# Optimization experiments

Measured on AMD Instinct MI355X. Metric: run time of the kernel, lower is better.

The kernel has to match this reference:

```python
import jax, jax.numpy as jnp
import numpy as np

K_NBR = 64  # max_num_neighbors in radius()
M1, M2, M3 = 2048, 512, 512  # fps sample counts: 4096*0.5, 2048*0.25, 512*1.0
R1, R2, R3 = 0.2, 0.4, 1.0


def _fps_idx(pos, m):
    # Furthest point sampling, deterministic start at index 0. pos: [N,3] -> idx [m]
    d2 = jnp.sum((pos - pos[0]) ** 2, axis=-1)  # [N]

    def step(min_d2, _):
        nxt = jnp.argmax(min_d2).astype(jnp.int32)
        min_d2 = jnp.minimum(min_d2, jnp.sum((pos - pos[nxt]) ** 2, axis=-1))
        return min_d2, nxt

    _, rest = jax.lax.scan(step, d2, None, length=m - 1)
    return jnp.concatenate([jnp.zeros((1,), jnp.int32), rest])


def _ball_query(pos_src, pos_q, r, k):
    # Nearest up-to-k neighbors within radius r. Returns idx [M,k], valid mask [M,k].
    d2 = (jnp.sum(pos_q ** 2, -1)[:, None] + jnp.sum(pos_src ** 2, -1)[None, :]
          - 2.0 * pos_q @ pos_src.T)  # [M,N]
    neg = jnp.where(d2 <= r * r, -d2, -jnp.inf)
    vals, idx = jax.lax.top_k(neg, k)
    return idx, vals > -jnp.inf


def _sa_layer(x, pos, m, r, w1, b1, w2, b2):
    # x: [B,N,C], pos: [B,N,3] -> (x_new [B,m,Cout], pos_new [B,m,3])
    idx = jax.vmap(lambda p: _fps_idx(p, m))(pos)                     # [B,m]
    pos_q = jnp.take_along_axis(pos, idx[..., None], axis=1)         # [B,m,3]
    nbr, mask = jax.vmap(lambda s, q: _ball_query(s, q, r, K_NBR))(pos, pos_q)
    gather = jax.vmap(lambda a, i: a[i])                              # [N,C],[m,k]->[m,k,C]
    x_j = gather(x, nbr)                                              # [B,m,k,C]
    pos_j = gather(pos, nbr)                                          # [B,m,k,3]
    # PointNetConv message: MLP(concat(x_j, pos_j - pos_i)), max-aggregate
    msg = jnp.concatenate([x_j, pos_j - pos_q[:, :, None, :]], axis=-1)
    h = jnp.maximum(msg @ w1 + b1, 0.0) @ w2 + b2                     # [B,m,k,Cout]
    h = jnp.where(mask[..., None], h, -jnp.inf)
    out = jnp.max(h, axis=2)
    out = jnp.where(jnp.any(mask, axis=2, keepdims=True), out, 0.0)   # empty -> 0
    return out, pos_q


def setup_inputs() -> dict:
    key = jax.random.key(0)
    ks = jax.random.split(key, 8)
    B, N, C3 = 8, 4096, 128
    pos = jax.random.uniform(ks[0], (B, N, 3), jnp.float32)
    batch = jnp.repeat(jnp.arange(B, dtype=jnp.int32)[:, None], N, axis=1)

    def lin(k, ci, co):
        kw, kb = jax.random.split(k)
        s = 1.0 / np.sqrt(ci)
        return (jax.random.uniform(kw, (ci, co), jnp.float32, -s, s),
                jax.random.uniform(kb, (co,), jnp.float32, -s, s))

    w11, b11 = lin(ks[1], 3 + 3, 32)
    w12, b12 = lin(ks[2], 32, 32)
    w21, b21 = lin(ks[3], 32 + 3, 64)
    w22, b22 = lin(ks[4], 64, 64)
    w31, b31 = lin(ks[5], 64 + 3, C3)
    w32, b32 = lin(ks[6], C3, C3)
    return dict(pos=pos, batch=batch,
                w11=w11, b11=b11, w12=w12, b12=b12,
                w21=w21, b21=b21, w22=w22, b22=b22,
                w31=w31, b31=b31, w32=w32, b32=b32)


def reference(pos, batch, w11, b11, w12, b12, w21, b21, w22, b22, w31, b31, w32, b32):
    # Layer 1 uses positions as features (x = pos in encoder forward)
    x1, p1 = _sa_layer(pos, pos, M1, R1, w11, b11, w12, b12)
    x2, p2 = _sa_layer(x1, p1, M2, R2, w21, b21, w22, b22)
    x3, p3 = _sa_layer(x2, p2, M3, R3, w31, b31, w32, b32)
    return x3, p3, batch[:, :M3]
```

## Files before the change

### kernel.cpp

```cpp
#include <hip/hip_runtime.h>
#include <hip/hip_bf16.h>
#include <float.h>

typedef unsigned long long u64;

static __device__ __forceinline__ float d2_rn(float ax, float ay, float az,
                                              float bx, float by, float bz) {
  float dx = __fsub_rn(ax, bx), dy = __fsub_rn(ay, by), dz = __fsub_rn(az, bz);
  return __fadd_rn(__fadd_rn(__fmul_rn(dx, dx), __fmul_rn(dy, dy)), __fmul_rn(dz, dz));
}

template<int CTRL>
static __device__ __forceinline__ float dpp_f32(float x) {
  return __int_as_float(__builtin_amdgcn_update_dpp(0, __float_as_int(x), CTRL, 0xF, 0xF, true));
}

template<int CTRL>
static __device__ __forceinline__ int dpp_min_i32(int x) {
  int b = __builtin_amdgcn_update_dpp(0x7fffffff, x, CTRL, 0xF, 0xF, false);
  return x < b ? x : b;
}

template<int CTRL>
static __device__ __forceinline__ void top2_step(float& v1, float& v2) {
  float b1 = dpp_f32<CTRL>(v1);
  float b2 = dpp_f32<CTRL>(v2);
  float m1 = fmaxf(v1, b1);
  float lo = fminf(v1, b1);
  v2 = fmaxf(lo, fmaxf(v2, b2));
  v1 = m1;
}

static __device__ __forceinline__ void wave_top2_vals(float& v1, float& v2) {
  top2_step<0xB1>(v1, v2);
  top2_step<0x4E>(v1, v2);
  top2_step<0x141>(v1, v2);
  top2_step<0x140>(v1, v2);
  top2_step<0x142>(v1, v2);
  top2_step<0x143>(v1, v2);
}

static __device__ __forceinline__ void pool_top2_vals(float& v1, float& v2) {
  top2_step<0xB1>(v1, v2);
  top2_step<0x4E>(v1, v2);
  top2_step<0x141>(v1, v2);
  top2_step<0x140>(v1, v2);
}

static __device__ __forceinline__ int wave_min_idx(int c) {
  c = dpp_min_i32<0xB1>(c);  c = dpp_min_i32<0x4E>(c);
  c = dpp_min_i32<0x141>(c); c = dpp_min_i32<0x140>(c);
  c = dpp_min_i32<0x142>(c); c = dpp_min_i32<0x143>(c);
  return __builtin_amdgcn_readlane(c, 63);
}

static __device__ __forceinline__ int pool_min_idx(int c) {
  c = dpp_min_i32<0xB1>(c);  c = dpp_min_i32<0x4E>(c);
  c = dpp_min_i32<0x141>(c); c = dpp_min_i32<0x140>(c);
  return __builtin_amdgcn_readfirstlane(c);
}

static __device__ __forceinline__ float readlane_f(float x, int l) {
  return __int_as_float(__builtin_amdgcn_readlane(__float_as_int(x), l));
}

static __device__ __forceinline__ void wave_recover_idx(float lv1, int li1, float lv2, int li2,
                                                        float s1, float s2, int lane,
                                                        int& i1g, int& i2g) {
  u64 b1 = __ballot(lv1 == s1);
  int lw;
  if (__popcll(b1) == 1) {
    lw = __ffsll(b1) - 1;
    i1g = __builtin_amdgcn_readlane(li1, lw);
  } else {
    i1g = wave_min_idx(lv1 == s1 ? li1 : 0x7fffffff);
    lw = __ffsll(__ballot(lv1 == s1 && li1 == i1g)) - 1;
  }
  float wlv = (lane == lw) ? lv2 : lv1;
  int   wli = (lane == lw) ? li2 : li1;
  u64 b2 = __ballot(wlv == s2);
  if (__popcll(b2) == 1) {
    i2g = __builtin_amdgcn_readlane(wli, __ffsll(b2) - 1);
  } else {
    i2g = wave_min_idx(wlv == s2 ? wli : 0x7fffffff);
  }
}

template<int N, int M, int NPT, int T>
static __device__ void fps_body(const float* __restrict__ P, float* __restrict__ O,
                                char* smem) {
  constexpr int W = T / 64;
  static_assert(N == T * NPT, "layout");
  float4* pq = (float4*)smem;
  uint4* slots = (uint4*)(pq + N);
  const int tid = threadIdx.x;
  const int lane = tid & 63, wv = tid >> 6;

  for (int j = tid; j < N; j += T)
    pq[j] = make_float4(P[3 * j], P[3 * j + 1], P[3 * j + 2], 0.f);
  __syncthreads();

  const float4 c0 = pq[0];
  if (tid == 0) { O[0] = c0.x; O[1] = c0.y; O[2] = c0.z; }

  float md[NPT], px[NPT], py[NPT], pz[NPT];
  float v1 = -1.f, v2 = -1.f; int i1 = 0, i2 = 0;
  #pragma unroll
  for (int k = 0; k < NPT; ++k) {
    int j = tid + k * T;
    float4 p = pq[j];
    px[k] = p.x; py[k] = p.y; pz[k] = p.z;
    float m = d2_rn(p.x, p.y, p.z, c0.x, c0.y, c0.z);
    md[k] = m;
    if (m > v2) { if (m > v1) { v2=v1; i2=i1; v1=m; i1=j; } else { v2=m; i2=j; } }
  }

  {
    float r1 = v1, r2 = v2;
    wave_top2_vals(r1, r2);
    float s1 = readlane_f(r1, 63), s2 = readlane_f(r2, 63);
    int i1g, i2g;
    wave_recover_idx(v1, i1, v2, i2, s1, s2, lane, i1g, i2g);
    if (lane == 0)
      slots[wv] = make_uint4(__float_as_uint(s1), (unsigned)i1g,
                             __float_as_uint(s2), (unsigned)i2g);
  }

  int t = 1, phase = 0;
  while (t < M) {
    __syncthreads();
    uint4 sp = slots[phase * W + (lane & (W - 1))];
    float pv; int pidx;
    if (lane & 8) { pv = __uint_as_float(sp.z); pidx = (int)sp.w; }
    else          { pv = __uint_as_float(sp.x); pidx = (int)sp.y; }
    const bool inp = lane < 16;
    if (!inp) { pv = -1.0f; pidx = 0x7fffffff; }
    float r1 = pv, r2 = -1.0f;
    pool_top2_vals(r1, r2);
    const float s1v = __int_as_float(__builtin_amdgcn_readfirstlane(__float_as_int(r1)));
    const float s2v = __int_as_float(__builtin_amdgcn_readfirstlane(__float_as_int(r2)));
    u64 b1 = __ballot(inp && pv == s1v);
    int lw, j1;
    if (__popcll(b1) == 1) {
      lw = __ffsll(b1) - 1;
      j1 = __builtin_amdgcn_readlane(pidx, lw);
    } else {
      j1 = pool_min_idx((inp && pv == s1v) ? pidx : 0x7fffffff);
      lw = __ffsll(__ballot(inp && pv == s1v && pidx == j1)) - 1;
    }
    float pw = (lane == lw) ? -1.0f : pv;
    int j2 = 0;
    u64 b2 = __ballot(inp && pw == s2v);
    if (__popcll(b2) == 1) j2 = __builtin_amdgcn_readlane(pidx, __ffsll(b2) - 1);
    else if (b2)           j2 = pool_min_idx((inp && pw == s2v) ? pidx : 0x7fffffff);

    const float4 c1 = pq[j1];
    const float v2f = s2v;

    bool hit = false;
    float4 c2 = make_float4(0.f, 0.f, 0.f, 0.f);
    if (t + 1 < M && v2f > 0.f) {
      c2 = pq[j2];
      float dd = d2_rn(c2.x, c2.y, c2.z, c1.x, c1.y, c1.z);
      hit = (dd >= v2f);
    }

    if (tid == 0) {
      O[3 * t] = c1.x; O[3 * t + 1] = c1.y; O[3 * t + 2] = c1.z;
      if (hit) { O[3 * t + 3] = c2.x; O[3 * t + 4] = c2.y; O[3 * t + 5] = c2.z; }
    }

    v1 = -1.f; v2 = -1.f; i1 = 0; i2 = 0;
    if (hit) {
      #pragma unroll
      for (int k = 0; k < NPT; ++k) {
        float m = md[k];
        m = fminf(m, d2_rn(px[k], py[k], pz[k], c1.x, c1.y, c1.z));
        m = fminf(m, d2_rn(px[k], py[k], pz[k], c2.x, c2.y, c2.z));
        md[k] = m;
        int j = tid + k * T;
        if (m > v2) { if (m > v1) { v2=v1; i2=i1; v1=m; i1=j; } else { v2=m; i2=j; } }
      }
    } else {
      #pragma unroll
      for (int k = 0; k < NPT; ++k) {
        float m = fminf(md[k], d2_rn(px[k], py[k], pz[k], c1.x, c1.y, c1.z));
        md[k] = m;
        int j = tid + k * T;
        if (m > v2) { if (m > v1) { v2=v1; i2=i1; v1=m; i1=j; } else { v2=m; i2=j; } }
      }
    }

    {
      float r1b = v1, r2b = v2;
      wave_top2_vals(r1b, r2b);
      float s1 = readlane_f(r1b, 63), s2 = readlane_f(r2b, 63);
      int i1g, i2g;
      wave_recover_idx(v1, i1, v2, i2, s1, s2, lane, i1g, i2g);
      if (lane == 0)
        slots[(phase ^ 1) * W + wv] = make_uint4(__float_as_uint(s1), (unsigned)i1g,
                                                 __float_as_uint(s2), (unsigned)i2g);
    }
    phase ^= 1;
    t += hit ? 2 : 1;
  }
}

template<int N, int M, int NPT>
__global__ __launch_bounds__(512, 2) void fps_kernel(const float* __restrict__ pos,
                                                     float* __restrict__ out) {
  __shared__ __align__(16) char smem[16 * N + 2 * 8 * 16];
  fps_body<N, M, NPT, 512>(pos + (size_t)blockIdx.x * N * 3,
                           out + (size_t)blockIdx.x * M * 3, smem);
}

template<int C, int H>
__global__ void g_kernel(const float* __restrict__ x, const float* __restrict__ pos,
                         const float* __restrict__ W, float* __restrict__ g, int rows) {
  int idx = blockIdx.x * 256 + threadIdx.x;
  if (idx >= rows * H) return;
  int row = idx / H, h = idx - row * H;
  const float* xr = x + (size_t)row * C;
  const float* pr = pos + (size_t)row * 3;
  float acc = 0.f;
  for (int c = 0; c < C; ++c) acc = fmaf(xr[c], W[c * H + h], acc);
  #pragma unroll
  for (int c = 0; c < 3; ++c) acc = fmaf(pr[c], W[(C + c) * H + h], acc);
  g[idx] = acc;
}

template<int N, int H, int C, int T>
constexpr int sa_smem_bytes() {
  constexpr int TPS = C / 2, SG = T / TPS, JT = SG * 4, STRIDE = JT + 4;
  constexpr int SCR = (SG * C > 512) ? SG * C : 512;
  return H * C * 2 + N * 4 + H * 4 + STRIDE * H * 4 + SCR * 4 + 64 * 4 + 8 * 4 + 8 * 4;
}

template<int N, int H, int C, int QB, int T>
static __device__ void sa_body(const float* __restrict__ srcb,
                               const float* __restrict__ gb,
                               const float* __restrict__ qposb,
                               const float* __restrict__ W2, const float* __restrict__ b1v,
                               const float* __restrict__ W1p, const float* __restrict__ b2v,
                               float r2, int M, float* __restrict__ outb, int qtile,
                               char* smem) {
  constexpr int TPS = C / 2;
  constexpr int SG  = T / TPS;
  constexpr int JT  = SG * 4;
  constexpr int STRIDE = JT + 4;
  constexpr int SCR = (SG * C > 512) ? SG * C : 512;
  const int tid = threadIdx.x;
  const int sgi = tid / TPS;
  const int c2 = 2 * (tid - sgi * TPS);

  __hip_bfloat16* sW2h = (__hip_bfloat16*)smem;
  float* sD2  = (float*)(smem + H * C * 2);
  float* sT   = sD2 + N;
  float* sHj  = sT + H;
  float* sScr = sHj + STRIDE * H;
  int*   sNbr = (int*)(sScr + SCR);
  int*   sWS  = sNbr + 64;
  int*   sIv  = sWS + 8;
  float* sFv  = (float*)(sIv + 6);

  int*   sHist  = (int*)sScr;
  float* sCand  = sScr + 256;
  int*   sCandI = (int*)(sScr + 320);
  float* sRed   = sScr;

  for (int e = tid; e < H * C; e += T) sW2h[e] = __float2bfloat16(W2[e]);

  for (int qi = 0; qi < QB; ++qi) {
    const int i = qtile * QB + qi;
    const float* qp = qposb + (size_t)i * 3;
    const float qx = qp[0], qy = qp[1], qz = qp[2];
    const float qq = __fadd_rn(__fadd_rn(__fmul_rn(qx, qx), __fmul_rn(qy, qy)),
                               __fmul_rn(qz, qz));
    if (tid < H)
      sT[tid] = fmaf(qx, W1p[tid], fmaf(qy, W1p[H + tid], fmaf(qz, W1p[2 * H + tid], -b1v[tid])));
    if (tid == 0) { sIv[0] = 0; sIv[1] = 0; sIv[2] = 0; }
    if (tid < 256) sHist[tid] = 0;
    __syncthreads();

    int lc = 0;
    for (int j = tid; j < N; j += T) {
      float sx = srcb[3 * j], sy = srcb[3 * j + 1], sz = srcb[3 * j + 2];
      float ss  = __fadd_rn(__fadd_rn(__fmul_rn(sx, sx), __fmul_rn(sy, sy)), __fmul_rn(sz, sz));
      float dot = __fadd_rn(__fadd_rn(__fmul_rn(qx, sx), __fmul_rn(qy, sy)), __fmul_rn(qz, sz));
      float d2  = __fsub_rn(__fadd_rn(qq, ss), __fmul_rn(2.0f, dot));
      sD2[j] = d2;
      lc += (d2 <= r2) ? 1 : 0;
    }
    #pragma unroll
    for (int off = 32; off > 0; off >>= 1) lc += __shfl_xor(lc, off, 64);
    if ((tid & 63) == 0) atomicAdd(&sIv[0], lc);
    __syncthreads();
    const int cnt = sIv[0];

    float tauv; int taui;
    if (cnt <= 64) {
      tauv = r2; taui = 0x7fffffff;
    } else {
      const float scale = 256.0f / r2;
      for (int j = tid; j < N; j += T) {
        float d2 = sD2[j];
        if (d2 <= r2) {
          int bin = (int)(d2 * scale);
          bin = bin < 0 ? 0 : (bin > 255 ? 255 : bin);
          atomicAdd(&sHist[bin], 1);
        }
      }
      __syncthreads();
      int cbin = (tid < 256) ? sHist[tid] : 0;
      int lane = tid & 63, wvi = tid >> 6;
      int v = cbin;
      #pragma unroll
      for (int off = 1; off < 64; off <<= 1) {
        int o = __shfl_up(v, off, 64);
        if (lane >= off) v += o;
      }
      if (lane == 63) sWS[wvi] = v;
      __syncthreads();
      int wadd = 0;
      for (int w = 0; w < wvi; ++w) wadd += sWS[w];
      int incl = v + wadd, excl = incl - cbin;
      if (tid < 256 && excl < 64 && incl >= 64) { sIv[3] = tid; sIv[4] = excl; }
      __syncthreads();
      const int bstar = sIv[3];
      const int kneed = 64 - sIv[4];
      for (int j = tid; j < N; j += T) {
        float d2 = sD2[j];
        if (d2 <= r2) {
          int bin = (int)(d2 * scale);
          bin = bin < 0 ? 0 : (bin > 255 ? 255 : bin);
          if (bin == bstar) {
            int p = atomicAdd(&sIv[2], 1);
            if (p < 64) { sCand[p] = d2; sCandI[p] = j; }
          }
        }
      }
      __syncthreads();
      if (tid == 0) {
        int nc = sIv[2] < 64 ? sIv[2] : 64;
        for (int a = 1; a < nc; ++a) {
          float dv = sCand[a]; int di = sCandI[a];
          int p = a - 1;
          while (p >= 0 && (sCand[p] > dv || (sCand[p] == dv && sCandI[p] > di))) {
            sCand[p + 1] = sCand[p]; sCandI[p + 1] = sCandI[p]; --p;
          }
          sCand[p + 1] = dv; sCandI[p + 1] = di;
        }
        int kk = (kneed < nc ? kneed : nc) - 1; if (kk < 0) kk = 0;
        sFv[0] = sCand[kk]; sIv[5] = sCandI[kk];
      }
      __syncthreads();
      tauv = sFv[0]; taui = sIv[5];
    }

    for (int j = tid; j < N; j += T) {
      float d2 = sD2[j];
      if (d2 < tauv || (d2 == tauv && j <= taui)) {
        int p = atomicAdd(&sIv[1], 1);
        if (p < 64) sNbr[p] = j;
      }
    }
    __syncthreads();
    const int nn = sIv[1] < 64 ? sIv[1] : 64;

    float m0 = -FLT_MAX, m1 = -FLT_MAX;
    for (int t0 = 0; t0 < nn; t0 += JT) {
      int jt = nn - t0; if (jt > JT) jt = JT;
      __syncthreads();
      for (int e = tid; e < JT * H; e += T) {
        int jj = e / H, h = e - jj * H;
        float hv = 0.f;
        if (jj < jt) {
          int j = sNbr[t0 + jj];
          hv = gb[(size_t)j * H + h] - sT[h];
          hv = hv > 0.f ? hv : 0.f;
        }
        sHj[h * STRIDE + jj] = hv;
      }
      __syncthreads();
      float a0 = 0, a1 = 0, a2 = 0, a3 = 0, c0 = 0, c1 = 0, c2a = 0, c3 = 0;
      const int jbase = sgi * 4;
      for (int h = 0; h < H; ++h) {
        float4 hv = *reinterpret_cast<const float4*>(&sHj[h * STRIDE + jbase]);
        __hip_bfloat162 wp = *reinterpret_cast<const __hip_bfloat162*>(&sW2h[h * C + c2]);
        float wx = __bfloat162float(wp.x), wy = __bfloat162float(wp.y);
        a0 = fmaf(hv.x, wx, a0); a1 = fmaf(hv.y, wx, a1);
        a2 = fmaf(hv.z, wx, a2); a3 = fmaf(hv.w, wx, a3);
        c0 = fmaf(hv.x, wy, c0); c1 = fmaf(hv.y, wy, c1);
        c2a = fmaf(hv.z, wy, c2a); c3 = fmaf(hv.w, wy, c3);
      }
      if (jbase + 0 < jt) { m0 = fmaxf(m0, a0); m1 = fmaxf(m1, c0); }
      if (jbase + 1 < jt) { m0 = fmaxf(m0, a1); m1 = fmaxf(m1, c1); }
      if (jbase + 2 < jt) { m0 = fmaxf(m0, a2); m1 = fmaxf(m1, c2a); }
      if (jbase + 3 < jt) { m0 = fmaxf(m0, a3); m1 = fmaxf(m1, c3); }
    }
    __syncthreads();
    sRed[sgi * C + c2]     = m0;
    sRed[sgi * C + c2 + 1] = m1;
    __syncthreads();
    if (tid < TPS) {
      int c = 2 * tid;
      float M0 = sRed[c], M1 = sRed[c + 1];
      #pragma unroll
      for (int s2 = 1; s2 < SG; ++s2) {
        M0 = fmaxf(M0, sRed[s2 * C + c]);
        M1 = fmaxf(M1, sRed[s2 * C + c + 1]);
      }
      float o0 = nn > 0 ? M0 + b2v[c]     : 0.f;
      float o1 = nn > 0 ? M1 + b2v[c + 1] : 0.f;
      float* orow = outb + (size_t)i * C;
      orow[c] = o0; orow[c + 1] = o1;
    }
    __syncthreads();
  }
}

template<int N, int H, int C, int QB>
__global__ __launch_bounds__(256) void sa_kernel(
    const float* __restrict__ src, const float* __restrict__ g,
    const float* __restrict__ qpos, const float* __restrict__ W2,
    const float* __restrict__ b1v, const float* __restrict__ W1p,
    const float* __restrict__ b2v, float r2, int M, float* __restrict__ out) {
  __shared__ __align__(16) char smem[sa_smem_bytes<N, H, C, 256>()];
  const int b = blockIdx.y;
  sa_body<N, H, C, QB, 256>(src + (size_t)b * N * 3, g + (size_t)b * N * H,
                            qpos + (size_t)b * M * 3, W2, b1v, W1p, b2v, r2, M,
                            out + (size_t)b * M * C, blockIdx.x, smem);
}

template<int NF, int MF, int NPTF, int NS, int HS, int CS, int QB, int SAB>
__global__ __launch_bounds__(512, 2) void fused_kernel(
    const float* __restrict__ fsrc, float* __restrict__ fdst,
    const float* __restrict__ src, const float* __restrict__ g,
    const float* __restrict__ qpos, const float* __restrict__ W2,
    const float* __restrict__ b1v, const float* __restrict__ W1p,
    const float* __restrict__ b2v, float r2, int M, float* __restrict__ out) {
  constexpr int FPS_BYTES = 16 * NF + 2 * 8 * 16;
  constexpr int SA_BYTES  = sa_smem_bytes<NS, HS, CS, 512>();
  constexpr int SMEM = FPS_BYTES > SA_BYTES ? FPS_BYTES : SA_BYTES;
  __shared__ __align__(16) char smem[SMEM];
  if (blockIdx.x < 8) {
    __builtin_amdgcn_s_setprio(3);
    fps_body<NF, MF, NPTF, 512>(fsrc + (size_t)blockIdx.x * NF * 3,
                                fdst + (size_t)blockIdx.x * MF * 3, smem);
    return;
  }
  const int bi = blockIdx.x - 8;
  const int qt = bi % SAB;
  const int b  = bi / SAB;
  sa_body<NS, HS, CS, QB, 512>(src + (size_t)b * NS * 3, g + (size_t)b * NS * HS,
                               qpos + (size_t)b * M * 3, W2, b1v, W1p, b2v, r2, M,
                               out + (size_t)b * M * CS, qt, smem);
}

__global__ void tail_kernel(const float* __restrict__ p3, float* __restrict__ d_out) {
  int i = blockIdx.x * 256 + threadIdx.x;
  if (i < 8 * 512 * 3) d_out[524288 + i] = p3[i];
  if (i < 8 * 512)     d_out[536576 + i] = (float)(i >> 9);
}

extern "C" void kernel_launch(void* const* d_in, const int* in_sizes, int n_in,
                              void* d_out, int out_size, void* d_ws, size_t ws_size,
                              hipStream_t stream) {
  (void)in_sizes; (void)n_in; (void)out_size; (void)ws_size;
  const float* pos = (const float*)d_in[0];
  const float* w11 = (const float*)d_in[2];
  const float* b11 = (const float*)d_in[3];
  const float* w12 = (const float*)d_in[4];
  const float* b12 = (const float*)d_in[5];
  const float* w21 = (const float*)d_in[6];
  const float* b21 = (const float*)d_in[7];
  const float* w22 = (const float*)d_in[8];
  const float* b22 = (const float*)d_in[9];
  const float* w31 = (const float*)d_in[10];
  const float* b31 = (const float*)d_in[11];
  const float* w32 = (const float*)d_in[12];
  const float* b32 = (const float*)d_in[13];

  float* ws = (float*)d_ws;
  float* p1 = ws; ws += 8 * 2048 * 3;
  float* p2 = ws; ws += 8 * 512 * 3;
  float* p3 = ws; ws += 8 * 512 * 3;
  float* g1 = ws; ws += 8 * 4096 * 32;
  float* x1 = ws; ws += 8 * 2048 * 32;
  float* g2 = ws; ws += 8 * 2048 * 64;
  float* x2 = ws; ws += 8 * 512 * 64;
  float* g3 = ws; ws += 8 * 512 * 128;
  float* x3 = (float*)d_out;

  g_kernel<3, 32><<<dim3(8 * 4096 * 32 / 256), dim3(256), 0, stream>>>(pos, pos, w11, g1, 8 * 4096);
  fps_kernel<4096, 2048, 8><<<dim3(8), dim3(512), 0, stream>>>(pos, p1);

  fused_kernel<2048, 512, 4, 4096, 32, 32, 8, 256><<<dim3(8 + 8 * 256), dim3(512), 0, stream>>>(
      p1, p2, pos, g1, p1, w12, b11, w11 + 3 * 32, b12, 0.04f, 2048, x1);

  g_kernel<32, 64><<<dim3(8 * 2048 * 64 / 256), dim3(256), 0, stream>>>(x1, p1, w21, g2, 8 * 2048);

  fused_kernel<512, 512, 1, 2048, 64, 64, 8, 64><<<dim3(8 + 8 * 64), dim3(512), 0, stream>>>(
      p2, p3, p1, g2, p2, w22, b21, w21 + 32 * 64, b22, 0.16f, 512, x2);

  g_kernel<64, 128><<<dim3(8 * 512 * 128 / 256), dim3(256), 0, stream>>>(x2, p2, w31, g3, 8 * 512);

  sa_kernel<512, 128, 128, 8><<<dim3(64, 8), dim3(256), 0, stream>>>(
      p2, g3, p3, w32, b31, w31 + 64 * 128, b32, 1.0f, 512, x3);

  tail_kernel<<<dim3(48), dim3(256), 0, stream>>>(p3, (float*)d_out);
}
```

Measured before the change: 2.185 ms.

## Accept up to four FPS centers per iteration using packed u64 top-2 merges

The FPS loop used to accept at most two new centers per barrier round, checking whether the second-best candidate stays farthest after the first is added. It now packs each value and its inverted index into one u64 key, which makes the pool reduction a single top-2 merge that also breaks ties. A second top-2 pass over the remaining wave candidates adds a third and fourth candidate, which are accepted when they stay at least as far from every earlier pick and come from distinct waves. The aim is fewer serial synchronized iterations, paid for with more reduction work per round and a min-update loop specialized for 1 to 4 centers through a switch.

```diff
diff --git a/kernel.cpp b/kernel.cpp
--- a/kernel.cpp
+++ b/kernel.cpp
@@ -19,6 +19,42 @@
 static __device__ __forceinline__ int dpp_min_i32(int x) {
   int b = __builtin_amdgcn_update_dpp(0x7fffffff, x, CTRL, 0xF, 0xF, false);
   return x < b ? x : b;
+}
+
+template<int CTRL>
+static __device__ __forceinline__ u64 dpp_u64(u64 x) {
+  unsigned lo = (unsigned)__builtin_amdgcn_update_dpp(0, (int)(unsigned)x, CTRL, 0xF, 0xF, true);
+  unsigned hi = (unsigned)__builtin_amdgcn_update_dpp(0, (int)(unsigned)(x >> 32), CTRL, 0xF, 0xF, true);
+  return ((u64)hi << 32) | lo;
+}
+
+static __device__ __forceinline__ void merge2(u64& a1, u64& a2, u64 b1, u64 b2) {
+  bool agt = a1 > b1;
+  u64 m1 = agt ? a1 : b1;
+  u64 lo = agt ? b1 : a1;
+  u64 cs = agt ? a2 : b2;
+  a1 = m1;
+  a2 = lo > cs ? lo : cs;
+}
+
+template<int CTRL>
+static __device__ __forceinline__ void merge_dpp(u64& a1, u64& a2) {
+  u64 b1 = dpp_u64<CTRL>(a1);
+  u64 b2 = dpp_u64<CTRL>(a2);
+  merge2(a1, a2, b1, b2);
+}
+
+static __device__ __forceinline__ void pool16_top2(u64& a1, u64& a2) {
+  merge_dpp<0xB1>(a1, a2);
+  merge_dpp<0x4E>(a1, a2);
+  merge_dpp<0x141>(a1, a2);
+  merge_dpp<0x140>(a1, a2);
+}
+
+static __device__ __forceinline__ u64 bcast64(u64 x) {
+  unsigned lo = (unsigned)__builtin_amdgcn_readfirstlane((int)(unsigned)x);
+  unsigned hi = (unsigned)__builtin_amdgcn_readfirstlane((int)(x >> 32));
+  return ((u64)hi << 32) | lo;
 }
 
 template<int CTRL>
@@ -40,24 +76,11 @@
   top2_step<0x143>(v1, v2);
 }
 
-static __device__ __forceinline__ void pool_top2_vals(float& v1, float& v2) {
-  top2_step<0xB1>(v1, v2);
-  top2_step<0x4E>(v1, v2);
-  top2_step<0x141>(v1, v2);
-  top2_step<0x140>(v1, v2);
-}
-
 static __device__ __forceinline__ int wave_min_idx(int c) {
   c = dpp_min_i32<0xB1>(c);  c = dpp_min_i32<0x4E>(c);
   c = dpp_min_i32<0x141>(c); c = dpp_min_i32<0x140>(c);
   c = dpp_min_i32<0x142>(c); c = dpp_min_i32<0x143>(c);
   return __builtin_amdgcn_readlane(c, 63);
-}
-
-static __device__ __forceinline__ int pool_min_idx(int c) {
-  c = dpp_min_i32<0xB1>(c);  c = dpp_min_i32<0x4E>(c);
-  c = dpp_min_i32<0x141>(c); c = dpp_min_i32<0x140>(c);
-  return __builtin_amdgcn_readfirstlane(c);
 }
 
 static __device__ __forceinline__ float readlane_f(float x, int l) {
@@ -86,6 +109,17 @@
   }
 }
 
+#define FPS_UPD(PP)                                                                    \
+  { _Pragma("unroll")                                                                  \
+    for (int k = 0; k < NPT; ++k) {                                                    \
+      float m = md[k];                                                                 \
+      _Pragma("unroll")                                                                \
+      for (int mm = 0; mm < (PP); ++mm)                                                \
+        m = fminf(m, d2_rn(px[k], py[k], pz[k], cx[mm], cy[mm], cz[mm]));              \
+      md[k] = m; int j = tid + k * T;                                                  \
+      if (m > v2) { if (m > v1) { v2=v1; i2=i1; v1=m; i1=j; } else { v2=m; i2=j; } }   \
+    } }
+
 template<int N, int M, int NPT, int T>
 static __device__ void fps_body(const float* __restrict__ P, float* __restrict__ O,
                                 char* smem) {
@@ -130,65 +164,81 @@
   while (t < M) {
     __syncthreads();
     uint4 sp = slots[phase * W + (lane & (W - 1))];
-    float pv; int pidx;
-    if (lane & 8) { pv = __uint_as_float(sp.z); pidx = (int)sp.w; }
-    else          { pv = __uint_as_float(sp.x); pidx = (int)sp.y; }
-    const bool inp = lane < 16;
-    if (!inp) { pv = -1.0f; pidx = 0x7fffffff; }
-    float r1 = pv, r2 = -1.0f;
-    pool_top2_vals(r1, r2);
-    const float s1v = __int_as_float(__builtin_amdgcn_readfirstlane(__float_as_int(r1)));
-    const float s2v = __int_as_float(__builtin_amdgcn_readfirstlane(__float_as_int(r2)));
-    u64 b1 = __ballot(inp && pv == s1v);
-    int lw, j1;
-    if (__popcll(b1) == 1) {
-      lw = __ffsll(b1) - 1;
-      j1 = __builtin_amdgcn_readlane(pidx, lw);
-    } else {
-      j1 = pool_min_idx((inp && pv == s1v) ? pidx : 0x7fffffff);
-      lw = __ffsll(__ballot(inp && pv == s1v && pidx == j1)) - 1;
-    }
-    float pw = (lane == lw) ? -1.0f : pv;
-    int j2 = 0;
-    u64 b2 = __ballot(inp && pw == s2v);
-    if (__popcll(b2) == 1) j2 = __builtin_amdgcn_readlane(pidx, __ffsll(b2) - 1);
-    else if (b2)           j2 = pool_min_idx((inp && pw == s2v) ? pidx : 0x7fffffff);
+    u64 key;
+    {
+      unsigned vb = (lane & 8) ? sp.z : sp.x;
+      unsigned ib = (lane & 8) ? sp.w : sp.y;
+      key = ((u64)vb << 32) | (unsigned)(~ib);
+    }
+    if (lane >= 16) key = 0;
+    u64 a1 = key, a2 = 0;
+    pool16_top2(a1, a2);
+    a1 = bcast64(a1); a2 = bcast64(a2);
+    const int j1 = (int)(~(unsigned)a1);
+    const int j2 = (int)(~(unsigned)a2);
+    const float v2f = __uint_as_float((unsigned)(a2 >> 32));
+    u64 b1 = (key == a1 || key == a2) ? 0ull : key, b2 = 0;
+    pool16_top2(b1, b2);
+    b1 = bcast64(b1); b2 = bcast64(b2);
 
     const float4 c1 = pq[j1];
-    const float v2f = s2v;
-
-    bool hit = false;
-    float4 c2 = make_float4(0.f, 0.f, 0.f, 0.f);
-    if (t + 1 < M && v2f > 0.f) {
-      c2 = pq[j2];
-      float dd = d2_rn(c2.x, c2.y, c2.z, c1.x, c1.y, c1.z);
-      hit = (dd >= v2f);
+    const float4 c2 = pq[j2];
+
+    const int room = M - t;
+    float cx[4], cy[4], cz[4];
+    cx[0] = c1.x; cy[0] = c1.y; cz[0] = c1.z;
+    int p = 1;
+    unsigned seen = 1u << ((j1 & (T - 1)) >> 6);
+    bool capped = false;
+    bool hit = (room >= 2) && (v2f > 0.f) &&
+               (d2_rn(c2.x, c2.y, c2.z, c1.x, c1.y, c1.z) >= v2f);
+    if (hit) {
+      cx[1] = c2.x; cy[1] = c2.y; cz[1] = c2.z; p = 2;
+      unsigned wb = 1u << ((j2 & (T - 1)) >> 6);
+      if (seen & wb) capped = true;
+      seen |= wb;
+      if (!capped && room >= 3) {
+        const float v3 = __uint_as_float((unsigned)(b1 >> 32));
+        if (v3 > 0.f) {
+          const int j3 = (int)(~(unsigned)b1);
+          const float4 c3 = pq[j3];
+          if (d2_rn(c3.x, c3.y, c3.z, c1.x, c1.y, c1.z) >= v3 &&
+              d2_rn(c3.x, c3.y, c3.z, c2.x, c2.y, c2.z) >= v3) {
+            cx[2] = c3.x; cy[2] = c3.y; cz[2] = c3.z; p = 3;
+            unsigned wb3 = 1u << ((j3 & (T - 1)) >> 6);
+            if (seen & wb3) capped = true;
+            seen |= wb3;
+            if (!capped && room >= 4) {
+              const float v4 = __uint_as_float((unsigned)(b2 >> 32));
+              if (v4 > 0.f) {
+                const int j4 = (int)(~(unsigned)b2);
+                const float4 c4 = pq[j4];
+                if (d2_rn(c4.x, c4.y, c4.z, c1.x, c1.y, c1.z) >= v4 &&
+                    d2_rn(c4.x, c4.y, c4.z, c2.x, c2.y, c2.z) >= v4 &&
+                    d2_rn(c4.x, c4.y, c4.z, c3.x, c3.y, c3.z) >= v4) {
+                  cx[3] = c4.x; cy[3] = c4.y; cz[3] = c4.z; p = 4;
+                }
+              }
+            }
+          }
+        }
+      }
     }
 
     if (tid == 0) {
-      O[3 * t] = c1.x; O[3 * t + 1] = c1.y; O[3 * t + 2] = c1.z;
-      if (hit) { O[3 * t + 3] = c2.x; O[3 * t + 4] = c2.y; O[3 * t + 5] = c2.z; }
+      #pragma unroll
+      for (int mm = 0; mm < 4; ++mm)
+        if (mm < p) {
+          O[3 * (t + mm)] = cx[mm]; O[3 * (t + mm) + 1] = cy[mm]; O[3 * (t + mm) + 2] = cz[mm];
+        }
     }
 
     v1 = -1.f; v2 = -1.f; i1 = 0; i2 = 0;
-    if (hit) {
-      #pragma unroll
-      for (int k = 0; k < NPT; ++k) {
-        float m = md[k];
-        m = fminf(m, d2_rn(px[k], py[k], pz[k], c1.x, c1.y, c1.z));
-        m = fminf(m, d2_rn(px[k], py[k], pz[k], c2.x, c2.y, c2.z));
-        md[k] = m;
-        int j = tid + k * T;
-        if (m > v2) { if (m > v1) { v2=v1; i2=i1; v1=m; i1=j; } else { v2=m; i2=j; } }
-      }
-    } else {
-      #pragma unroll
-      for (int k = 0; k < NPT; ++k) {
-        float m = fminf(md[k], d2_rn(px[k], py[k], pz[k], c1.x, c1.y, c1.z));
-        md[k] = m;
-        int j = tid + k * T;
-        if (m > v2) { if (m > v1) { v2=v1; i2=i1; v1=m; i1=j; } else { v2=m; i2=j; } }
-      }
+    switch (p) {
+      case 1:  FPS_UPD(1); break;
+      case 2:  FPS_UPD(2); break;
+      case 3:  FPS_UPD(3); break;
+      default: FPS_UPD(4); break;
     }
 
     {
@@ -202,7 +252,7 @@
                                                  __float_as_uint(s2), (unsigned)i2g);
     }
     phase ^= 1;
-    t += hit ? 2 : 1;
+    t += p;
   }
 }
 
```

Measured after the change: 2.188 ms. Within noise of the previous version (+0.2%).
